# Optimization experiments

Hardware: AMD Instinct MI355X
Metric: run time of the kernel (lower is better)

Reference implementation:

```python
import jax, jax.numpy as jnp
import numpy as np

NH_CA, DH_CA = 8, 32          # channel-attention heads / dim_head (inner=256)
NH_CS = 8                      # cswin heads
SPLIT = 4                      # cswin split_size
DIM = 128


def conv1x1(t, w):
    # t: [b,c,h,w], w: [o,c]
    return jnp.einsum('bchw,oc->bohw', t, w)


def to_windows(t, p1, p2, heads):
    # 'b (h d) (x p1) (y p2) -> (b x y) h (p1 p2) d'
    b, c, H, W = t.shape
    d = c // heads
    xb, yb = H // p1, W // p2
    t = t.reshape(b, heads, d, xb, p1, yb, p2)
    t = t.transpose(0, 3, 5, 1, 4, 6, 2)
    return t.reshape(b * xb * yb, heads, p1 * p2, d)


def from_windows(t, b, p1, p2, H, W, heads):
    # '(b x y) h (p1 p2) d -> b (h d) (x p1) (y p2)'
    xb, yb = H // p1, W // p2
    d = t.shape[-1]
    t = t.reshape(b, xb, yb, heads, p1, p2, d)
    t = t.transpose(0, 3, 6, 1, 4, 2, 5)
    return t.reshape(b, heads * d, H, W)


def channel_attention(x, temp, qkv_w, proj_w):
    b, c, H, W = x.shape
    qkv = conv1x1(x, qkv_w)                        # [b, 3*inner, H, W]
    q, k, v = jnp.split(qkv, 3, axis=1)
    hd = lambda t: t.reshape(b, NH_CA, DH_CA, H * W)
    q, k, v = hd(q), hd(k), hd(v)
    # L2-normalize over spatial axis
    nrm = lambda t: t / jnp.maximum(jnp.sqrt(jnp.sum(t * t, axis=-1, keepdims=True)), 1e-12)
    q, k = nrm(q), nrm(k)
    attn = jnp.einsum('bhcn,bhdn->bhcd', q, k) * temp   # [b,h,32,32]
    attn = jax.nn.softmax(attn, axis=-1)
    out = jnp.einsum('bhcd,bhdn->bhcn', attn, v)
    out = out.reshape(b, NH_CA * DH_CA, H, W)
    return conv1x1(out, proj_w)


def cswin(fmap, qk_w, v_w, vv_w, vh_w, proj_w):
    b, n, H, W = fmap.shape
    half = n // 2
    scale = (n // NH_CS) ** -0.5
    qk = conv1x1(fmap, qk_w)
    q_all, k_all = jnp.split(qk, 2, axis=1)
    v_all = conv1x1(fmap, v_w)
    q_h, q_v = q_all[:, :half], q_all[:, half:]
    k_h, k_v = k_all[:, :half], k_all[:, half:]
    v_h, v_v = v_all[:, :half], v_all[:, half:]
    # vertical LePE uses conv; horizontal LePE is (faithfully) the raw v_h
    # due to the overwrite bug in the original source; vh_w is unused math.
    v_v_lepe = conv1x1(v_v, vv_w)
    v_h_lepe = v_h

    def attend(q, k, v, lepe, p1, p2):
        qw = to_windows(q, p1, p2, NH_CS) * scale
        kw = to_windows(k, p1, p2, NH_CS)
        vw = to_windows(v, p1, p2, NH_CS)
        lw = to_windows(lepe, p1, p2, NH_CS)
        attn = jax.nn.softmax(jnp.einsum('whqd,whkd->whqk', qw, kw), axis=-1)
        o = jnp.einsum('whqk,whkd->whqd', attn, vw) + lw
        return from_windows(o, b, p1, p2, H, W, NH_CS)

    out_h = attend(q_h, k_h, v_h, v_h_lepe, H, SPLIT)      # horizontal strips
    out_v = attend(q_v, k_v, v_v, v_v_lepe, SPLIT, W)      # vertical strips
    return fmap + conv1x1(jnp.concatenate([out_h, out_v], axis=1), proj_w)


def setup_inputs() -> dict:
    key = jax.random.key(0)
    ks = jax.random.split(key, 9)
    s = 0.05
    return {
        'x': jax.random.normal(ks[0], (16, DIM, 64, 64), jnp.float32),
        'ca_temp': jnp.ones((NH_CA, 1, 1), jnp.float32),
        'ca_qkv_w': jax.random.normal(ks[1], (3 * NH_CA * DH_CA, DIM), jnp.float32) * s,
        'ca_proj_w': jax.random.normal(ks[2], (DIM, NH_CA * DH_CA), jnp.float32) * s,
        'cs_qk_w': jax.random.normal(ks[3], (2 * DIM, DIM), jnp.float32) * s,
        'cs_v_w': jax.random.normal(ks[4], (DIM, DIM), jnp.float32) * s,
        'cs_vv_w': jax.random.normal(ks[5], (DIM // 2, DIM // 2), jnp.float32) * s,
        'cs_vh_w': jax.random.normal(ks[6], (DIM // 2, DIM // 2), jnp.float32) * s,
        'cs_proj_w': jax.random.normal(ks[7], (DIM, DIM), jnp.float32) * s,
    }


def reference(x, ca_temp, ca_qkv_w, ca_proj_w, cs_qk_w, cs_v_w, cs_vv_w, cs_vh_w, cs_proj_w):
    x = x + channel_attention(x, ca_temp, ca_qkv_w, ca_proj_w)
    return cswin(x, cs_qk_w, cs_v_w, cs_vv_w, cs_vh_w, cs_proj_w)
```

## Files before the change

kernel.cpp:

```cpp
#include <hip/hip_runtime.h>
#include <cstdint>

#define NPOS 4096
#define CHT  768
#define NB   16

__global__ __launch_bounds__(256)
void gemm_k(const float* __restrict__ A, const float* __restrict__ B,
            const float* __restrict__ R, float* __restrict__ C,
            int K, int64_t sB, int64_t sR, int64_t sC)
{
    const int tid = threadIdx.x;
    const int b   = blockIdx.z;
    const int n0  = blockIdx.x * 64;
    const int o0  = blockIdx.y * 64;
    const float* Bb = B + (int64_t)b * sB;

    __shared__ float As[32][68];
    __shared__ float Bs[32][64];

    const int tm = tid >> 4;
    const int tn = tid & 15;
    float acc[4][4] = {};

    const int ar = tid >> 3;
    const int ak = (tid & 7) << 2;
    const int br = tid >> 4;
    const int bn = (tid & 15) << 2;

    for (int k0 = 0; k0 < K; k0 += 32) {
        #pragma unroll
        for (int p = 0; p < 2; p++) {
            int r = ar + p * 32;
            float4 a4 = *(const float4*)&A[(int64_t)(o0 + r) * K + k0 + ak];
            As[ak + 0][r] = a4.x; As[ak + 1][r] = a4.y;
            As[ak + 2][r] = a4.z; As[ak + 3][r] = a4.w;
        }
        #pragma unroll
        for (int p = 0; p < 2; p++) {
            int r = br + p * 16;
            *(float4*)&Bs[r][bn] = *(const float4*)&Bb[(int64_t)(k0 + r) * NPOS + n0 + bn];
        }
        __syncthreads();
        #pragma unroll 8
        for (int kk = 0; kk < 32; kk++) {
            float4 a4 = *(const float4*)&As[kk][tm*4];
            float4 b4 = *(const float4*)&Bs[kk][tn*4];
            acc[0][0] += a4.x*b4.x; acc[0][1] += a4.x*b4.y; acc[0][2] += a4.x*b4.z; acc[0][3] += a4.x*b4.w;
            acc[1][0] += a4.y*b4.x; acc[1][1] += a4.y*b4.y; acc[1][2] += a4.y*b4.z; acc[1][3] += a4.y*b4.w;
            acc[2][0] += a4.z*b4.x; acc[2][1] += a4.z*b4.y; acc[2][2] += a4.z*b4.z; acc[2][3] += a4.z*b4.w;
            acc[3][0] += a4.w*b4.x; acc[3][1] += a4.w*b4.y; acc[3][2] += a4.w*b4.z; acc[3][3] += a4.w*b4.w;
        }
        __syncthreads();
    }

    float* Cb = C + (int64_t)b * sC;
    #pragma unroll
    for (int i = 0; i < 4; i++) {
        int o = o0 + tm * 4 + i;
        float4 v = make_float4(acc[i][0], acc[i][1], acc[i][2], acc[i][3]);
        if (R) {
            const float* Rb = R + (int64_t)b * sR;
            float4 r4 = *(const float4*)&Rb[(int64_t)o * NPOS + n0 + tn*4];
            v.x += r4.x; v.y += r4.y; v.z += r4.z; v.w += r4.w;
        }
        *(float4*)&Cb[(int64_t)o * NPOS + n0 + tn*4] = v;
    }
}

__global__ __launch_bounds__(256)
void ca_partial_k(const float* __restrict__ qkv, float* __restrict__ part)
{
    const int chunk = blockIdx.x;
    const int bh = blockIdx.y;
    const int b = bh >> 3, h = bh & 7;
    const float* Q  = qkv + ((int64_t)b * CHT + h * 32) * NPOS;
    const float* Kp = qkv + ((int64_t)b * CHT + 256 + h * 32) * NPOS;

    __shared__ float Qs[32][68], Ks[32][68];
    __shared__ float nrm[2][32][8];

    const int tid = threadIdx.x;
    const int c  = tid & 31;
    const int dq = tid >> 5;
    float s[4] = {0.f, 0.f, 0.f, 0.f};
    float sqp = 0.f, skp = 0.f;

    const int lr = tid >> 4;
    const int lc = (tid & 15) << 2;

    const int nbase = chunk * 512;
    for (int nc0 = nbase; nc0 < nbase + 512; nc0 += 64) {
        #pragma unroll
        for (int p = 0; p < 2; p++) {
            int r = lr + p * 16;
            *(float4*)&Qs[r][lc] = *(const float4*)&Q [(int64_t)r * NPOS + nc0 + lc];
            *(float4*)&Ks[r][lc] = *(const float4*)&Kp[(int64_t)r * NPOS + nc0 + lc];
        }
        __syncthreads();
        #pragma unroll
        for (int kk = 0; kk < 64; kk += 4) {
            float4 qv = *(const float4*)&Qs[c][kk];
            #pragma unroll
            for (int j = 0; j < 4; j++) {
                float4 kv = *(const float4*)&Ks[dq*4+j][kk];
                s[j] += qv.x*kv.x + qv.y*kv.y + qv.z*kv.z + qv.w*kv.w;
            }
        }
        #pragma unroll
        for (int kk = dq*8; kk < dq*8+8; kk += 4) {
            float4 qv = *(const float4*)&Qs[c][kk];
            float4 kv = *(const float4*)&Ks[c][kk];
            sqp += qv.x*qv.x + qv.y*qv.y + qv.z*qv.z + qv.w*qv.w;
            skp += kv.x*kv.x + kv.y*kv.y + kv.z*kv.z + kv.w*kv.w;
        }
        __syncthreads();
    }

    float* pp = part + ((int64_t)bh * 8 + chunk) * 1088;
    #pragma unroll
    for (int j = 0; j < 4; j++)
        pp[(dq*4+j)*32 + c] = s[j];

    nrm[0][c][dq] = sqp;
    nrm[1][c][dq] = skp;
    __syncthreads();
    if (tid < 64) {
        int row = tid & 31, which = tid >> 5;
        float acc = 0.f;
        #pragma unroll
        for (int p = 0; p < 8; p++) acc += nrm[which][row][p];
        pp[1024 + which*32 + row] = acc;
    }
}

__global__ __launch_bounds__(256)
void ca_reduce_k(const float* __restrict__ part, const float* __restrict__ temp,
                 float* __restrict__ attn)
{
    const int bh = blockIdx.x;
    const int h = bh & 7;
    const float* pp = part + (int64_t)bh * 8 * 1088;

    __shared__ float Ss[1024];
    __shared__ float nq[32], nk[32];

    const int tid = threadIdx.x;
    {
        float4 acc = make_float4(0.f, 0.f, 0.f, 0.f);
        #pragma unroll
        for (int p = 0; p < 8; p++) {
            float4 v = *(const float4*)&pp[p*1088 + tid*4];
            acc.x += v.x; acc.y += v.y; acc.z += v.z; acc.w += v.w;
        }
        *(float4*)&Ss[tid*4] = acc;
    }
    if (tid < 64) {
        int row = tid & 31, which = tid >> 5;
        float a = 0.f;
        #pragma unroll
        for (int p = 0; p < 8; p++) a += pp[p*1088 + 1024 + which*32 + row];
        float n = fmaxf(sqrtf(a), 1e-12f);
        if (which == 0) nq[row] = n; else nk[row] = n;
    }
    __syncthreads();

    if (tid < 32) {
        const int cc = tid;
        float tn_ = temp[h] / nq[cc];
        float vals[32];
        float mx = -1e30f;
        #pragma unroll
        for (int d = 0; d < 32; d++) {
            float v = Ss[d*32 + cc] * tn_ / nk[d];
            vals[d] = v;
            mx = fmaxf(mx, v);
        }
        float sum = 0.f;
        #pragma unroll
        for (int d = 0; d < 32; d++) { vals[d] = __expf(vals[d] - mx); sum += vals[d]; }
        float inv = 1.f / sum;
        float* ap = attn + ((int64_t)bh * 32 + cc) * 32;
        #pragma unroll
        for (int d = 0; d < 32; d++) ap[d] = vals[d] * inv;
    }
}

__global__ __launch_bounds__(256)
void ca_av_k(const float* __restrict__ qkv, const float* __restrict__ attn,
             float* __restrict__ outp)
{
    const int bh = blockIdx.y, b = bh >> 3, h = bh & 7;
    const float* V = qkv + ((int64_t)b * CHT + 512 + h * 32) * NPOS;
    float* O = outp + ((int64_t)b * CHT + h * 32) * NPOS;

    __shared__ float As[1024];
    ((float4*)As)[threadIdx.x] = ((const float4*)(attn + (int64_t)bh * 1024))[threadIdx.x & 255];
    __syncthreads();

    const int n = blockIdx.x * 256 + threadIdx.x;
    float acc[32];
    #pragma unroll
    for (int c = 0; c < 32; c++) acc[c] = 0.f;

    #pragma unroll 2
    for (int d0 = 0; d0 < 32; d0 += 4) {
        float v0 = V[(int64_t)(d0+0) * NPOS + n];
        float v1 = V[(int64_t)(d0+1) * NPOS + n];
        float v2 = V[(int64_t)(d0+2) * NPOS + n];
        float v3 = V[(int64_t)(d0+3) * NPOS + n];
        #pragma unroll
        for (int c = 0; c < 32; c++) {
            float4 a = *(const float4*)&As[c * 32 + d0];
            acc[c] += a.x * v0 + a.y * v1 + a.z * v2 + a.w * v3;
        }
    }
    #pragma unroll
    for (int c = 0; c < 32; c++) O[(int64_t)c * NPOS + n] = acc[c];
}

template<int HORIZ>
__global__ __launch_bounds__(256)
void cswin_k(float* __restrict__ base, int64_t qOff, int64_t kOff, int64_t vOff,
             int64_t lOff, int64_t oOff)
{
    const float SCALE = 0.25f;
    const int wnd = blockIdx.x, b = blockIdx.y, h = blockIdx.z;
    const int64_t bb = (int64_t)b * (CHT * NPOS) + (int64_t)h * 8 * NPOS;
    const float* Qp = base + bb + qOff;
    const float* Kp = base + bb + kOff;
    const float* Vp = base + bb + vOff;
    const float* Lp = base + bb + lOff;
    float*       Op = base + bb + oOff;

    const int t = threadIdx.x;
    int pos;
    if (HORIZ) pos = (t >> 2) * 64 + wnd * 4 + (t & 3);
    else       pos = (wnd * 4 + (t >> 6)) * 64 + (t & 63);

    __shared__ float Ks[8][260], Vs[8][260];
    __shared__ float wmax[4];
    float q[8];
    float qn = 0.f, kn = 0.f;
    #pragma unroll
    for (int ch = 0; ch < 8; ch++) {
        float kv = Kp[(int64_t)ch * NPOS + pos];
        Ks[ch][t] = kv; kn += kv * kv;
        Vs[ch][t] = Vp[(int64_t)ch * NPOS + pos];
        float qv = Qp[(int64_t)ch * NPOS + pos] * SCALE;
        q[ch] = qv; qn += qv * qv;
    }
    float knr = sqrtf(kn);
    #pragma unroll
    for (int o = 32; o > 0; o >>= 1) knr = fmaxf(knr, __shfl_xor(knr, o));
    if ((t & 63) == 0) wmax[t >> 6] = knr;
    __syncthreads();
    const float kmax = fmaxf(fmaxf(wmax[0], wmax[1]), fmaxf(wmax[2], wmax[3]));
    const float B = sqrtf(qn) * kmax;

    float l = 0.f;
    float acc[8];
    #pragma unroll
    for (int ch = 0; ch < 8; ch++) acc[ch] = 0.f;

    for (int k = 0; k < 256; k += 4) {
        float s0 = 0.f, s1 = 0.f, s2 = 0.f, s3 = 0.f;
        #pragma unroll
        for (int ch = 0; ch < 8; ch++) {
            float4 kv = *(const float4*)&Ks[ch][k];
            s0 += q[ch] * kv.x; s1 += q[ch] * kv.y;
            s2 += q[ch] * kv.z; s3 += q[ch] * kv.w;
        }
        float p0 = __expf(s0 - B), p1 = __expf(s1 - B);
        float p2 = __expf(s2 - B), p3 = __expf(s3 - B);
        l += (p0 + p1) + (p2 + p3);
        #pragma unroll
        for (int ch = 0; ch < 8; ch++) {
            float4 vv = *(const float4*)&Vs[ch][k];
            acc[ch] += p0 * vv.x + p1 * vv.y + p2 * vv.z + p3 * vv.w;
        }
    }
    float inv = 1.f / l;
    #pragma unroll
    for (int ch = 0; ch < 8; ch++)
        Op[(int64_t)ch * NPOS + pos] = acc[ch] * inv + Lp[(int64_t)ch * NPOS + pos];
}

extern "C" void kernel_launch(void* const* d_in, const int* in_sizes, int n_in,
                              void* d_out, int out_size, void* d_ws, size_t ws_size,
                              hipStream_t stream)
{
    (void)in_sizes; (void)n_in; (void)out_size; (void)ws_size;
    const float* x         = (const float*)d_in[0];
    const float* ca_temp   = (const float*)d_in[1];
    const float* ca_qkv_w  = (const float*)d_in[2];
    const float* ca_proj_w = (const float*)d_in[3];
    const float* cs_qk_w   = (const float*)d_in[4];
    const float* cs_v_w    = (const float*)d_in[5];
    const float* cs_vv_w   = (const float*)d_in[6];
    const float* cs_proj_w = (const float*)d_in[8];
    float* out = (float*)d_out;

    float* buf  = (float*)d_ws;
    float* x1   = buf + (int64_t)NB * CHT * NPOS;
    float* attn = x1 + (int64_t)NB * 128 * NPOS;
    float* part = x1;

    const int64_t SB = (int64_t)CHT * NPOS;
    const int64_t SX = (int64_t)128 * NPOS;
    dim3 blk(256);

    gemm_k<<<dim3(64, 12, NB), blk, 0, stream>>>(ca_qkv_w, x, nullptr, buf, 128, SX, 0, SB);
    ca_partial_k<<<dim3(8, 128), blk, 0, stream>>>(buf, part);
    ca_reduce_k<<<dim3(128), blk, 0, stream>>>(part, ca_temp, attn);
    ca_av_k<<<dim3(16, 128), blk, 0, stream>>>(buf, attn, buf);
    gemm_k<<<dim3(64, 2, NB), blk, 0, stream>>>(ca_proj_w, buf, x, x1, 256, SB, SX, SX);
    gemm_k<<<dim3(64, 4, NB), blk, 0, stream>>>(cs_qk_w, x1, nullptr, buf, 128, SX, 0, SB);
    gemm_k<<<dim3(64, 2, NB), blk, 0, stream>>>(cs_v_w,  x1, nullptr, buf + (int64_t)256 * NPOS, 128, SX, 0, SB);
    gemm_k<<<dim3(64, 1, NB), blk, 0, stream>>>(cs_vv_w, buf + (int64_t)320 * NPOS, nullptr,
                                                buf + (int64_t)384 * NPOS, 64, SB, 0, SB);
    cswin_k<1><<<dim3(16, NB, 8), blk, 0, stream>>>(buf, (int64_t)0,          (int64_t)128 * NPOS,
                                                    (int64_t)256 * NPOS, (int64_t)256 * NPOS,
                                                    (int64_t)448 * NPOS);
    cswin_k<0><<<dim3(16, NB, 8), blk, 0, stream>>>(buf, (int64_t)64 * NPOS,  (int64_t)192 * NPOS,
                                                    (int64_t)320 * NPOS, (int64_t)384 * NPOS,
                                                    (int64_t)512 * NPOS);
    gemm_k<<<dim3(64, 2, NB), blk, 0, stream>>>(cs_proj_w, buf + (int64_t)448 * NPOS, x1, out,
                                                128, SB, SX, SX);
}
```

Before: 815.6 us.

## Rewrite channel attention via input Gram matrix and fold projection into one GEMM

```diff
diff --git a/kernel.cpp b/kernel.cpp
--- a/kernel.cpp
+++ b/kernel.cpp
@@ -2,221 +2,268 @@
 #include <cstdint>
 
 #define NPOS 4096
-#define CHT  768
+#define CHB  576
 #define NB   16
 
 __global__ __launch_bounds__(256)
-void gemm_k(const float* __restrict__ A, const float* __restrict__ B,
-            const float* __restrict__ R, float* __restrict__ C,
-            int K, int64_t sB, int64_t sR, int64_t sC)
-{
-    const int tid = threadIdx.x;
-    const int b   = blockIdx.z;
-    const int n0  = blockIdx.x * 64;
-    const int o0  = blockIdx.y * 64;
+void gemm128(const float* __restrict__ A, const float* __restrict__ B,
+             const float* __restrict__ R, float* __restrict__ C,
+             int K, int64_t ldB, int64_t ldC,
+             int64_t sA, int64_t sB, int64_t sR, int64_t sC)
+{
+    const int t  = threadIdx.x;
+    const int b  = blockIdx.z;
+    const int n0 = blockIdx.x * 128;
+    const int o0 = blockIdx.y * 64;
+    const float* Ab = A + (int64_t)b * sA;
     const float* Bb = B + (int64_t)b * sB;
 
     __shared__ float As[32][68];
-    __shared__ float Bs[32][64];
-
-    const int tm = tid >> 4;
-    const int tn = tid & 15;
-    float acc[4][4] = {};
-
-    const int ar = tid >> 3;
-    const int ak = (tid & 7) << 2;
-    const int br = tid >> 4;
-    const int bn = (tid & 15) << 2;
+    __shared__ float Bs[32][132];
+
+    const int to = t & 7;
+    const int tn = t >> 3;
+    float acc[8][4] = {};
+
+    const int ar = t & 31;
+    const int ak = (t >> 5) << 2;
+    const int bn = (t & 31) << 2;
+    const int br = t >> 5;
 
     for (int k0 = 0; k0 < K; k0 += 32) {
         #pragma unroll
         for (int p = 0; p < 2; p++) {
-            int r = ar + p * 32;
-            float4 a4 = *(const float4*)&A[(int64_t)(o0 + r) * K + k0 + ak];
+            int r = ar + 32 * p;
+            float4 a4 = *(const float4*)&Ab[(int64_t)(o0 + r) * K + k0 + ak];
             As[ak + 0][r] = a4.x; As[ak + 1][r] = a4.y;
             As[ak + 2][r] = a4.z; As[ak + 3][r] = a4.w;
         }
         #pragma unroll
-        for (int p = 0; p < 2; p++) {
-            int r = br + p * 16;
-            *(float4*)&Bs[r][bn] = *(const float4*)&Bb[(int64_t)(k0 + r) * NPOS + n0 + bn];
+        for (int p = 0; p < 4; p++) {
+            int r = br + 8 * p;
+            *(float4*)&Bs[r][bn] = *(const float4*)&Bb[(int64_t)(k0 + r) * ldB + n0 + bn];
         }
         __syncthreads();
-        #pragma unroll 8
+        #pragma unroll 4
         for (int kk = 0; kk < 32; kk++) {
-            float4 a4 = *(const float4*)&As[kk][tm*4];
-            float4 b4 = *(const float4*)&Bs[kk][tn*4];
-            acc[0][0] += a4.x*b4.x; acc[0][1] += a4.x*b4.y; acc[0][2] += a4.x*b4.z; acc[0][3] += a4.x*b4.w;
-            acc[1][0] += a4.y*b4.x; acc[1][1] += a4.y*b4.y; acc[1][2] += a4.y*b4.z; acc[1][3] += a4.y*b4.w;
-            acc[2][0] += a4.z*b4.x; acc[2][1] += a4.z*b4.y; acc[2][2] += a4.z*b4.z; acc[2][3] += a4.z*b4.w;
-            acc[3][0] += a4.w*b4.x; acc[3][1] += a4.w*b4.y; acc[3][2] += a4.w*b4.z; acc[3][3] += a4.w*b4.w;
+            float a[8];
+            *(float4*)&a[0] = *(const float4*)&As[kk][to * 8];
+            *(float4*)&a[4] = *(const float4*)&As[kk][to * 8 + 4];
+            float4 b4 = *(const float4*)&Bs[kk][tn * 4];
+            #pragma unroll
+            for (int i = 0; i < 8; i++) {
+                acc[i][0] += a[i] * b4.x; acc[i][1] += a[i] * b4.y;
+                acc[i][2] += a[i] * b4.z; acc[i][3] += a[i] * b4.w;
+            }
         }
         __syncthreads();
     }
 
     float* Cb = C + (int64_t)b * sC;
-    #pragma unroll
-    for (int i = 0; i < 4; i++) {
-        int o = o0 + tm * 4 + i;
+    const float* Rb = R ? (R + (int64_t)b * sR) : nullptr;
+    #pragma unroll
+    for (int i = 0; i < 8; i++) {
+        int o = o0 + to * 8 + i;
         float4 v = make_float4(acc[i][0], acc[i][1], acc[i][2], acc[i][3]);
-        if (R) {
-            const float* Rb = R + (int64_t)b * sR;
-            float4 r4 = *(const float4*)&Rb[(int64_t)o * NPOS + n0 + tn*4];
+        if (Rb) {
+            float4 r4 = *(const float4*)&Rb[(int64_t)o * ldC + n0 + tn * 4];
             v.x += r4.x; v.y += r4.y; v.z += r4.z; v.w += r4.w;
         }
-        *(float4*)&Cb[(int64_t)o * NPOS + n0 + tn*4] = v;
-    }
-}
-
-__global__ __launch_bounds__(256)
-void ca_partial_k(const float* __restrict__ qkv, float* __restrict__ part)
-{
-    const int chunk = blockIdx.x;
-    const int bh = blockIdx.y;
-    const int b = bh >> 3, h = bh & 7;
-    const float* Q  = qkv + ((int64_t)b * CHT + h * 32) * NPOS;
-    const float* Kp = qkv + ((int64_t)b * CHT + 256 + h * 32) * NPOS;
-
-    __shared__ float Qs[32][68], Ks[32][68];
-    __shared__ float nrm[2][32][8];
-
-    const int tid = threadIdx.x;
-    const int c  = tid & 31;
-    const int dq = tid >> 5;
-    float s[4] = {0.f, 0.f, 0.f, 0.f};
-    float sqp = 0.f, skp = 0.f;
-
-    const int lr = tid >> 4;
-    const int lc = (tid & 15) << 2;
-
-    const int nbase = chunk * 512;
-    for (int nc0 = nbase; nc0 < nbase + 512; nc0 += 64) {
-        #pragma unroll
-        for (int p = 0; p < 2; p++) {
-            int r = lr + p * 16;
-            *(float4*)&Qs[r][lc] = *(const float4*)&Q [(int64_t)r * NPOS + nc0 + lc];
-            *(float4*)&Ks[r][lc] = *(const float4*)&Kp[(int64_t)r * NPOS + nc0 + lc];
+        *(float4*)&Cb[(int64_t)o * ldC + n0 + tn * 4] = v;
+    }
+}
+
+__global__ __launch_bounds__(256)
+void gram_k(const float* __restrict__ x, float* __restrict__ P)
+{
+    const int chunk = blockIdx.x, b = blockIdx.y;
+    const float* X = x + (int64_t)b * 128 * NPOS;
+
+    __shared__ float Xs[32][132];
+    const int t  = threadIdx.x;
+    const int ti = t >> 4, tj = t & 15;
+    float acc[8][8] = {};
+
+    const int lc = t >> 3;
+    const int ln = (t & 7) << 2;
+
+    for (int k0 = 0; k0 < 128; k0 += 32) {
+        const int nbase = chunk * 128 + k0;
+        #pragma unroll
+        for (int p = 0; p < 4; p++) {
+            int c = lc + 32 * p;
+            float4 v = *(const float4*)&X[(int64_t)c * NPOS + nbase + ln];
+            Xs[ln + 0][c] = v.x; Xs[ln + 1][c] = v.y;
+            Xs[ln + 2][c] = v.z; Xs[ln + 3][c] = v.w;
         }
         __syncthreads();
-        #pragma unroll
-        for (int kk = 0; kk < 64; kk += 4) {
-            float4 qv = *(const float4*)&Qs[c][kk];
+        #pragma unroll 2
+        for (int kk = 0; kk < 32; kk++) {
+            float a[8], c8[8];
+            *(float4*)&a[0]  = *(const float4*)&Xs[kk][ti * 8];
+            *(float4*)&a[4]  = *(const float4*)&Xs[kk][ti * 8 + 4];
+            *(float4*)&c8[0] = *(const float4*)&Xs[kk][tj * 8];
+            *(float4*)&c8[4] = *(const float4*)&Xs[kk][tj * 8 + 4];
             #pragma unroll
-            for (int j = 0; j < 4; j++) {
-                float4 kv = *(const float4*)&Ks[dq*4+j][kk];
-                s[j] += qv.x*kv.x + qv.y*kv.y + qv.z*kv.z + qv.w*kv.w;
-            }
-        }
-        #pragma unroll
-        for (int kk = dq*8; kk < dq*8+8; kk += 4) {
-            float4 qv = *(const float4*)&Qs[c][kk];
-            float4 kv = *(const float4*)&Ks[c][kk];
-            sqp += qv.x*qv.x + qv.y*qv.y + qv.z*qv.z + qv.w*qv.w;
-            skp += kv.x*kv.x + kv.y*kv.y + kv.z*kv.z + kv.w*kv.w;
+            for (int i = 0; i < 8; i++)
+                #pragma unroll
+                for (int j = 0; j < 8; j++)
+                    acc[i][j] += a[i] * c8[j];
         }
         __syncthreads();
     }
 
-    float* pp = part + ((int64_t)bh * 8 + chunk) * 1088;
-    #pragma unroll
-    for (int j = 0; j < 4; j++)
-        pp[(dq*4+j)*32 + c] = s[j];
-
-    nrm[0][c][dq] = sqp;
-    nrm[1][c][dq] = skp;
-    __syncthreads();
-    if (tid < 64) {
-        int row = tid & 31, which = tid >> 5;
-        float acc = 0.f;
-        #pragma unroll
-        for (int p = 0; p < 8; p++) acc += nrm[which][row][p];
-        pp[1024 + which*32 + row] = acc;
-    }
-}
-
-__global__ __launch_bounds__(256)
-void ca_reduce_k(const float* __restrict__ part, const float* __restrict__ temp,
-                 float* __restrict__ attn)
-{
-    const int bh = blockIdx.x;
-    const int h = bh & 7;
-    const float* pp = part + (int64_t)bh * 8 * 1088;
-
-    __shared__ float Ss[1024];
-    __shared__ float nq[32], nk[32];
-
-    const int tid = threadIdx.x;
+    float* pp = P + (int64_t)(b * 32 + chunk) * 16384;
+    #pragma unroll
+    for (int i = 0; i < 8; i++) {
+        *(float4*)&pp[(ti * 8 + i) * 128 + tj * 8]     = *(float4*)&acc[i][0];
+        *(float4*)&pp[(ti * 8 + i) * 128 + tj * 8 + 4] = *(float4*)&acc[i][4];
+    }
+}
+
+__global__ __launch_bounds__(256)
+void gram_reduce_k(const float* __restrict__ P, float* __restrict__ G)
+{
+    const int b = blockIdx.y;
+    const int e = blockIdx.x * 256 + threadIdx.x;
+    float s = 0.f;
+    #pragma unroll 8
+    for (int c = 0; c < 32; c++) s += P[(int64_t)(b * 32 + c) * 16384 + e];
+    G[(int64_t)b * 16384 + e] = s;
+}
+
+__global__ __launch_bounds__(256)
+void ca_small_k(const float* __restrict__ G, const float* __restrict__ qkv_w,
+                const float* __restrict__ temp, float* __restrict__ AWv)
+{
+    const int h = blockIdx.x, b = blockIdx.y;
+    const float* Gb = G + (int64_t)b * 16384;
+
+    __shared__ float Wa[32][129];
+    __shared__ float Wb[32][129];
+    __shared__ float Tmp[32][129];
+    __shared__ float Ss[32][33];
+    __shared__ float nqp[32][8], nkp[32][8];
+    __shared__ float nk[32];
+
+    const int t = threadIdx.x;
+    const int r  = t & 31;
+    const int cg = t >> 5;
+
+    #pragma unroll
+    for (int j = 0; j < 4; j++) {
+        int col = cg * 16 + j * 4;
+        *(float4*)&Wa[r][col] = *(const float4*)&qkv_w[(int64_t)(h * 32 + r) * 128 + col];
+        *(float4*)&Wb[r][col] = *(const float4*)&qkv_w[(int64_t)(256 + h * 32 + r) * 128 + col];
+    }
+    __syncthreads();
+
     {
-        float4 acc = make_float4(0.f, 0.f, 0.f, 0.f);
-        #pragma unroll
-        for (int p = 0; p < 8; p++) {
-            float4 v = *(const float4*)&pp[p*1088 + tid*4];
-            acc.x += v.x; acc.y += v.y; acc.z += v.z; acc.w += v.w;
-        }
-        *(float4*)&Ss[tid*4] = acc;
-    }
-    if (tid < 64) {
-        int row = tid & 31, which = tid >> 5;
-        float a = 0.f;
-        #pragma unroll
-        for (int p = 0; p < 8; p++) a += pp[p*1088 + 1024 + which*32 + row];
-        float n = fmaxf(sqrtf(a), 1e-12f);
-        if (which == 0) nq[row] = n; else nk[row] = n;
-    }
-    __syncthreads();
-
-    if (tid < 32) {
-        const int cc = tid;
-        float tn_ = temp[h] / nq[cc];
-        float vals[32];
-        float mx = -1e30f;
+        float acc[16];
+        #pragma unroll
+        for (int u = 0; u < 16; u++) acc[u] = 0.f;
+        #pragma unroll 2
+        for (int i = 0; i < 128; i++) {
+            float w = Wb[r][i];
+            const float* g = &Gb[i * 128 + cg * 16];
+            float4 g0 = *(const float4*)&g[0],  g1 = *(const float4*)&g[4];
+            float4 g2 = *(const float4*)&g[8],  g3 = *(const float4*)&g[12];
+            acc[0] += w*g0.x; acc[1] += w*g0.y; acc[2] += w*g0.z; acc[3] += w*g0.w;
+            acc[4] += w*g1.x; acc[5] += w*g1.y; acc[6] += w*g1.z; acc[7] += w*g1.w;
+            acc[8] += w*g2.x; acc[9] += w*g2.y; acc[10]+= w*g2.z; acc[11]+= w*g2.w;
+            acc[12]+= w*g3.x; acc[13]+= w*g3.y; acc[14]+= w*g3.z; acc[15]+= w*g3.w;
+        }
+        float np = 0.f;
+        #pragma unroll
+        for (int u = 0; u < 16; u++) {
+            Tmp[r][cg * 16 + u] = acc[u];
+            np += acc[u] * Wb[r][cg * 16 + u];
+        }
+        nkp[r][cg] = np;
+    }
+    __syncthreads();
+    if (t < 32) {
+        float s = 0.f;
+        #pragma unroll
+        for (int p = 0; p < 8; p++) s += nkp[t][p];
+        nk[t] = fmaxf(sqrtf(s), 1e-12f);
+    }
+    {
+        #pragma unroll
+        for (int j = 0; j < 4; j++) {
+            int d = cg * 4 + j;
+            float s = 0.f;
+            #pragma unroll 4
+            for (int i = 0; i < 128; i++) s += Tmp[d][i] * Wa[r][i];
+            Ss[r][d] = s;
+        }
+    }
+    __syncthreads();
+
+    {
+        float acc[16];
+        #pragma unroll
+        for (int u = 0; u < 16; u++) acc[u] = 0.f;
+        #pragma unroll 2
+        for (int i = 0; i < 128; i++) {
+            float w = Wa[r][i];
+            const float* g = &Gb[i * 128 + cg * 16];
+            float4 g0 = *(const float4*)&g[0],  g1 = *(const float4*)&g[4];
+            float4 g2 = *(const float4*)&g[8],  g3 = *(const float4*)&g[12];
+            acc[0] += w*g0.x; acc[1] += w*g0.y; acc[2] += w*g0.z; acc[3] += w*g0.w;
+            acc[4] += w*g1.x; acc[5] += w*g1.y; acc[6] += w*g1.z; acc[7] += w*g1.w;
+            acc[8] += w*g2.x; acc[9] += w*g2.y; acc[10]+= w*g2.z; acc[11]+= w*g2.w;
+            acc[12]+= w*g3.x; acc[13]+= w*g3.y; acc[14]+= w*g3.z; acc[15]+= w*g3.w;
+        }
+        float np = 0.f;
+        #pragma unroll
+        for (int u = 0; u < 16; u++) np += acc[u] * Wa[r][cg * 16 + u];
+        nqp[r][cg] = np;
+        #pragma unroll
+        for (int j = 0; j < 4; j++) {
+            int col = cg * 16 + j * 4;
+            *(float4*)&Wb[r][col] = *(const float4*)&qkv_w[(int64_t)(512 + h * 32 + r) * 128 + col];
+        }
+    }
+    __syncthreads();
+
+    if (t < 32) {
+        const int c = t;
+        float s = 0.f;
+        #pragma unroll
+        for (int p = 0; p < 8; p++) s += nqp[c][p];
+        float nqc = fmaxf(sqrtf(s), 1e-12f);
+        float tn_ = temp[h] / nqc;
+        float vals[32], mx = -1e30f;
         #pragma unroll
         for (int d = 0; d < 32; d++) {
-            float v = Ss[d*32 + cc] * tn_ / nk[d];
-            vals[d] = v;
-            mx = fmaxf(mx, v);
+            float v = Ss[c][d] * tn_ / nk[d];
+            vals[d] = v; mx = fmaxf(mx, v);
         }
         float sum = 0.f;
         #pragma unroll
         for (int d = 0; d < 32; d++) { vals[d] = __expf(vals[d] - mx); sum += vals[d]; }
         float inv = 1.f / sum;
-        float* ap = attn + ((int64_t)bh * 32 + cc) * 32;
-        #pragma unroll
-        for (int d = 0; d < 32; d++) ap[d] = vals[d] * inv;
-    }
-}
-
-__global__ __launch_bounds__(256)
-void ca_av_k(const float* __restrict__ qkv, const float* __restrict__ attn,
-             float* __restrict__ outp)
-{
-    const int bh = blockIdx.y, b = bh >> 3, h = bh & 7;
-    const float* V = qkv + ((int64_t)b * CHT + 512 + h * 32) * NPOS;
-    float* O = outp + ((int64_t)b * CHT + h * 32) * NPOS;
-
-    __shared__ float As[1024];
-    ((float4*)As)[threadIdx.x] = ((const float4*)(attn + (int64_t)bh * 1024))[threadIdx.x & 255];
-    __syncthreads();
-
-    const int n = blockIdx.x * 256 + threadIdx.x;
-    float acc[32];
-    #pragma unroll
-    for (int c = 0; c < 32; c++) acc[c] = 0.f;
-
-    #pragma unroll 2
-    for (int d0 = 0; d0 < 32; d0 += 4) {
-        float v0 = V[(int64_t)(d0+0) * NPOS + n];
-        float v1 = V[(int64_t)(d0+1) * NPOS + n];
-        float v2 = V[(int64_t)(d0+2) * NPOS + n];
-        float v3 = V[(int64_t)(d0+3) * NPOS + n];
-        #pragma unroll
-        for (int c = 0; c < 32; c++) {
-            float4 a = *(const float4*)&As[c * 32 + d0];
-            acc[c] += a.x * v0 + a.y * v1 + a.z * v2 + a.w * v3;
-        }
-    }
-    #pragma unroll
-    for (int c = 0; c < 32; c++) O[(int64_t)c * NPOS + n] = acc[c];
+        #pragma unroll
+        for (int d = 0; d < 32; d++) Ss[c][d] = vals[d] * inv;
+    }
+    __syncthreads();
+
+    {
+        float acc[16];
+        #pragma unroll
+        for (int u = 0; u < 16; u++) acc[u] = 0.f;
+        #pragma unroll 4
+        for (int d = 0; d < 32; d++) {
+            float a = Ss[r][d];
+            #pragma unroll
+            for (int u = 0; u < 16; u++) acc[u] += a * Wb[d][cg * 16 + u];
+        }
+        float* op = AWv + (int64_t)b * 32768 + (int64_t)(h * 32 + r) * 128 + cg * 16;
+        #pragma unroll
+        for (int j = 0; j < 4; j++)
+            *(float4*)&op[j * 4] = make_float4(acc[j*4], acc[j*4+1], acc[j*4+2], acc[j*4+3]);
+    }
 }
 
 template<int HORIZ>
@@ -226,7 +273,7 @@
 {
     const float SCALE = 0.25f;
     const int wnd = blockIdx.x, b = blockIdx.y, h = blockIdx.z;
-    const int64_t bb = (int64_t)b * (CHT * NPOS) + (int64_t)h * 8 * NPOS;
+    const int64_t bb = (int64_t)b * (CHB * NPOS) + (int64_t)h * 8 * NPOS;
     const float* Qp = base + bb + qOff;
     const float* Kp = base + bb + kOff;
     const float* Vp = base + bb + vOff;
@@ -301,30 +348,38 @@
     const float* cs_proj_w = (const float*)d_in[8];
     float* out = (float*)d_out;
 
-    float* buf  = (float*)d_ws;
-    float* x1   = buf + (int64_t)NB * CHT * NPOS;
-    float* attn = x1 + (int64_t)NB * 128 * NPOS;
-    float* part = x1;
-
-    const int64_t SB = (int64_t)CHT * NPOS;
+    float* buf   = (float*)d_ws;
+    float* gramP = buf;
+    float* x1    = buf + (int64_t)NB * CHB * NPOS;
+    float* G     = x1 + (int64_t)NB * 128 * NPOS;
+    float* AWv   = G + (int64_t)NB * 16384;
+    float* M     = AWv + (int64_t)NB * 32768;
+
     const int64_t SX = (int64_t)128 * NPOS;
+    const int64_t SB2 = (int64_t)CHB * NPOS;
     dim3 blk(256);
 
-    gemm_k<<<dim3(64, 12, NB), blk, 0, stream>>>(ca_qkv_w, x, nullptr, buf, 128, SX, 0, SB);
-    ca_partial_k<<<dim3(8, 128), blk, 0, stream>>>(buf, part);
-    ca_reduce_k<<<dim3(128), blk, 0, stream>>>(part, ca_temp, attn);
-    ca_av_k<<<dim3(16, 128), blk, 0, stream>>>(buf, attn, buf);
-    gemm_k<<<dim3(64, 2, NB), blk, 0, stream>>>(ca_proj_w, buf, x, x1, 256, SB, SX, SX);
-    gemm_k<<<dim3(64, 4, NB), blk, 0, stream>>>(cs_qk_w, x1, nullptr, buf, 128, SX, 0, SB);
-    gemm_k<<<dim3(64, 2, NB), blk, 0, stream>>>(cs_v_w,  x1, nullptr, buf + (int64_t)256 * NPOS, 128, SX, 0, SB);
-    gemm_k<<<dim3(64, 1, NB), blk, 0, stream>>>(cs_vv_w, buf + (int64_t)320 * NPOS, nullptr,
-                                                buf + (int64_t)384 * NPOS, 64, SB, 0, SB);
+    gram_k<<<dim3(32, NB), blk, 0, stream>>>(x, gramP);
+    gram_reduce_k<<<dim3(64, NB), blk, 0, stream>>>(gramP, G);
+    ca_small_k<<<dim3(8, NB), blk, 0, stream>>>(G, ca_qkv_w, ca_temp, AWv);
+    gemm128<<<dim3(1, 2, NB), blk, 0, stream>>>(ca_proj_w, AWv, nullptr, M,
+                                                256, 128, 128, 0, 32768, 0, 16384);
+    gemm128<<<dim3(32, 2, NB), blk, 0, stream>>>(M, x, x, x1,
+                                                 128, NPOS, NPOS, 16384, SX, SX, SX);
+
+    gemm128<<<dim3(32, 4, NB), blk, 0, stream>>>(cs_qk_w, x1, nullptr, buf,
+                                                 128, NPOS, NPOS, 0, SX, 0, SB2);
+    gemm128<<<dim3(32, 2, NB), blk, 0, stream>>>(cs_v_w, x1, nullptr, buf + (int64_t)256 * NPOS,
+                                                 128, NPOS, NPOS, 0, SX, 0, SB2);
+    gemm128<<<dim3(32, 1, NB), blk, 0, stream>>>(cs_vv_w, buf + (int64_t)320 * NPOS, nullptr,
+                                                 buf + (int64_t)384 * NPOS,
+                                                 64, NPOS, NPOS, 0, SB2, 0, SB2);
     cswin_k<1><<<dim3(16, NB, 8), blk, 0, stream>>>(buf, (int64_t)0,          (int64_t)128 * NPOS,
                                                     (int64_t)256 * NPOS, (int64_t)256 * NPOS,
                                                     (int64_t)448 * NPOS);
     cswin_k<0><<<dim3(16, NB, 8), blk, 0, stream>>>(buf, (int64_t)64 * NPOS,  (int64_t)192 * NPOS,
                                                     (int64_t)320 * NPOS, (int64_t)384 * NPOS,
                                                     (int64_t)512 * NPOS);
-    gemm_k<<<dim3(64, 2, NB), blk, 0, stream>>>(cs_proj_w, buf + (int64_t)448 * NPOS, x1, out,
-                                                128, SB, SX, SX);
-}
+    gemm128<<<dim3(32, 2, NB), blk, 0, stream>>>(cs_proj_w, buf + (int64_t)448 * NPOS, x1, out,
+                                                 128, NPOS, NPOS, 0, SB2, SX, SX);
+}
```

Result: faster. 668.9 us (-18.0%).
